# Kernel tuning notes

Hardware: AMD Instinct MI355X
Metric: run time of the kernel (lower is better)

## Reference

```python
import jax, jax.numpy as jnp
import numpy as np

B, N, D = 8, 1024, 256
H, U = 8, 64  # num_heads, units per head


def setup_inputs() -> dict:
    key = jax.random.key(0)
    ks = jax.random.split(key, 8)
    X = jax.random.normal(ks[0], (B, N, D), dtype=jnp.float32)
    A = (jax.random.uniform(ks[1], (B, N, N)) < 0.1).astype(jnp.float32)
    A = jnp.maximum(A, jnp.eye(N, dtype=jnp.float32)[None])
    s = 1.0 / np.sqrt(D)
    kernel = jax.random.normal(ks[2], (D, H * U), dtype=jnp.float32) * s
    kernel_residual = jax.random.normal(ks[3], (D, H * U), dtype=jnp.float32) * s
    su = 1.0 / np.sqrt(U)
    attn_kernel_self = jax.random.normal(ks[4], (H, U, 1), dtype=jnp.float32) * su
    attn_kernel_neighs = jax.random.normal(ks[5], (H, U, 1), dtype=jnp.float32) * su
    bias = jnp.zeros((H * U,), dtype=jnp.float32)
    return {
        "X": X, "A": A,
        "kernel": kernel, "kernel_residual": kernel_residual,
        "attn_kernel_self": attn_kernel_self,
        "attn_kernel_neighs": attn_kernel_neighs,
        "bias": bias,
    }


def reference(X, A, kernel, kernel_residual, attn_kernel_self, attn_kernel_neighs, bias):
    # feature projections: [B,N,H*U]
    features = X @ kernel
    features_residual = X @ kernel_residual
    f = features.reshape(B, N, H, U)  # bnhu
    # additive attention logits per head
    attn_self = jnp.einsum('bnhu,hu->bnh', f, attn_kernel_self[..., 0])
    attn_neigh = jnp.einsum('bnhu,hu->bnh', f, attn_kernel_neighs[..., 0])
    dense = attn_self[:, :, None, :] + attn_neigh[:, None, :, :]  # b n k h
    dense = jax.nn.leaky_relu(dense, negative_slope=0.2)
    # mask non-edges, softmax over neighbor axis k
    dense = dense + (-1e10) * (1.0 - A)[..., None]
    attn_coef = jax.nn.softmax(dense, axis=2)
    # (dropout is identity in inference mode)
    node_features = jnp.einsum('bnkh,bkhu->bnhu', attn_coef, f)
    node_features = node_features.reshape(B, N, H * U) + features_residual + bias
    # head_reduction == 'concat' -> keep [B,N,H*U]
    return jax.nn.relu(node_features)
```

## Files before the change

kernel.cpp:

```cpp
#include <hip/hip_runtime.h>
#include <stdint.h>


typedef __attribute__((ext_vector_type(8))) short short8;
typedef __attribute__((ext_vector_type(4))) float f32x4;
struct __align__(8) us4 { unsigned short x, y, z, w; };

__device__ __forceinline__ unsigned short f32_to_bf16(float f) {
    unsigned int u = __float_as_uint(f);
    u = (u + 0x7fffu + ((u >> 16) & 1u)) >> 16;
    return (unsigned short)u;
}
__device__ __forceinline__ float bf16_to_f32(unsigned short s) {
    return __uint_as_float(((unsigned int)s) << 16);
}
__device__ __forceinline__ void load_lds16(const unsigned short* g, unsigned short* l) {
    __builtin_amdgcn_global_load_lds(
        (const __attribute__((address_space(1))) unsigned int*)g,
        (__attribute__((address_space(3))) unsigned int*)l, 16, 0, 0);
}

__global__ __launch_bounds__(256) void pack_a(const float* __restrict__ X,
                                              unsigned short* __restrict__ Abig) {
    const int idx = blockIdx.x * 256 + threadIdx.x;
    const int m  = idx >> 6;
    const int kg = (idx & 63) << 2;
    float4 x = *(const float4*)&X[m * 256 + kg];
    const float xs[4] = {x.x, x.y, x.z, x.w};
    union { unsigned short u[4]; uint64_t q; } hq, lq;
    #pragma unroll
    for (int i = 0; i < 4; i++) {
        unsigned short h = f32_to_bf16(xs[i]);
        hq.u[i] = h;
        lq.u[i] = f32_to_bf16(xs[i] - bf16_to_f32(h));
    }
    unsigned short* r = Abig + (size_t)m * 768;
    *(uint64_t*)(r + kg)       = hq.q;
    *(uint64_t*)(r + 256 + kg) = hq.q;
    *(uint64_t*)(r + 512 + kg) = lq.q;
}

__global__ __launch_bounds__(256) void pack_b(const float* __restrict__ Wk,
                                              const float* __restrict__ Wr,
                                              unsigned short* __restrict__ Bpack) {
    const int idx = blockIdx.x * 256 + threadIdx.x;
    const int n = idx / 768;
    const int k = idx - n * 768;
    const float* __restrict__ W = (n < 512) ? Wk : Wr;
    const int nc = n & 511;
    const float w = W[(k & 255) * 512 + nc];
    unsigned short h = f32_to_bf16(w);
    unsigned short o = (k >= 256 && k < 512) ? f32_to_bf16(w - bf16_to_f32(h)) : h;
    Bpack[idx] = o;
}

__global__ __launch_bounds__(512) void attn_ck(const float* __restrict__ kernel,
                                               const float* __restrict__ aks,
                                               const float* __restrict__ akn,
                                               float* __restrict__ ck) {
    const int d = blockIdx.x, j = threadIdx.x;
    const float kv = kernel[d * 512 + j];
    float a = kv * aks[j];
    float b = kv * akn[j];
    #pragma unroll
    for (int m = 32; m; m >>= 1) { a += __shfl_xor(a, m, 64); b += __shfl_xor(b, m, 64); }
    const int lane = j & 63, h = j >> 6;
    if (lane == 0) { ck[d * 16 + h] = a; ck[d * 16 + 8 + h] = b; }
}

__global__ __launch_bounds__(256) void attn_sa(const float* __restrict__ X,
                                               const float* __restrict__ ck,
                                               float* __restrict__ saan) {
    __shared__ __align__(16) float Xs[16][260];
    __shared__ __align__(16) float ckL[4096];
    const int t = threadIdx.x, row0 = blockIdx.x * 16;
    #pragma unroll
    for (int i = 0; i < 4; i++) {
        const int q = t + i * 256;
        const int r = q >> 6, c4 = (q & 63) * 4;
        *(float4*)&Xs[r][c4] = *(const float4*)&X[(size_t)(row0 + r) * 256 + c4];
        *(float4*)&ckL[q * 4] = *(const float4*)&ck[q * 4];
    }
    __syncthreads();
    const int r = t >> 4, o = t & 15;
    float acc = 0.f;
    #pragma unroll 4
    for (int d = 0; d < 256; d++) acc = fmaf(Xs[r][d], ckL[d * 16 + o], acc);
    saan[(size_t)(row0 + r) * 16 + o] = acc;
}

#define GK 768
__global__ __launch_bounds__(256) void gemm_bf16(const unsigned short* __restrict__ Ab,
                                                 const unsigned short* __restrict__ Bp,
                                                 unsigned short* __restrict__ featb,
                                                 float* __restrict__ outr) {
    __shared__ __align__(16) unsigned short As[128 * 32];
    __shared__ __align__(16) unsigned short Bs[128 * 32];
    const int tid = threadIdx.x;
    const int lane = tid & 63, wave = tid >> 6;
    const int wr = wave >> 1, wc = wave & 1;
    const int m0 = blockIdx.x * 128, n0 = blockIdx.y * 128;
    const int l15 = lane & 15, lhi = lane >> 4;

    f32x4 acc[4][4] = {};

    for (int k0 = 0; k0 < GK; k0 += 32) {
        #pragma unroll
        for (int i = 0; i < 2; i++) {
            const int s = tid + i * 256;
            const int row = s >> 2, kc = (s & 3) * 8;
            load_lds16(Ab + (size_t)(m0 + row) * GK + k0 + kc, &As[s * 8]);
            load_lds16(Bp + (size_t)(n0 + row) * GK + k0 + kc, &Bs[s * 8]);
        }
        asm volatile("s_waitcnt vmcnt(0)" ::: "memory");
        __syncthreads();
        short8 a[4], b[4];
        #pragma unroll
        for (int mi = 0; mi < 4; mi++)
            a[mi] = *(const short8*)&As[(wr * 64 + mi * 16 + l15) * 32 + lhi * 8];
        #pragma unroll
        for (int ni = 0; ni < 4; ni++)
            b[ni] = *(const short8*)&Bs[(wc * 64 + ni * 16 + l15) * 32 + lhi * 8];
        #pragma unroll
        for (int mi = 0; mi < 4; mi++)
            #pragma unroll
            for (int ni = 0; ni < 4; ni++)
                acc[mi][ni] = __builtin_amdgcn_mfma_f32_16x16x32_bf16(a[mi], b[ni], acc[mi][ni], 0, 0, 0);
        __syncthreads();
    }

    if (n0 < 512) {
        #pragma unroll
        for (int mi = 0; mi < 4; mi++)
            #pragma unroll
            for (int ni = 0; ni < 4; ni++) {
                const int col = n0 + wc * 64 + ni * 16 + l15;
                const int rbase = m0 + wr * 64 + mi * 16 + lhi * 4;
                #pragma unroll
                for (int r = 0; r < 4; r++)
                    featb[(size_t)(rbase + r) * 512 + col] = f32_to_bf16(acc[mi][ni][r]);
            }
    } else {
        #pragma unroll
        for (int mi = 0; mi < 4; mi++)
            #pragma unroll
            for (int ni = 0; ni < 4; ni++) {
                const int col = (n0 - 512) + wc * 64 + ni * 16 + l15;
                const int rbase = m0 + wr * 64 + mi * 16 + lhi * 4;
                #pragma unroll
                for (int r = 0; r < 4; r++)
                    outr[(size_t)(rbase + r) * 512 + col] = acc[mi][ni][r];
            }
    }
}

#define CAP 256
__global__ __launch_bounds__(512) void gat_row4(
    const float* __restrict__ A, const unsigned short* __restrict__ featb,
    const float* __restrict__ saan, const float* __restrict__ bias,
    float* __restrict__ out) {
    __shared__ int   elist[4][CAP];
    __shared__ float ew[4][CAP * 8];
    __shared__ float as_s[4][8], inv_s[4][8], wred[4][2][8];
    __shared__ int   cnt[4];

    const int row0 = blockIdx.x * 4, b = row0 >> 10, t = threadIdx.x;
    const int g = t >> 7, tl = t & 127;

    if (t < 4) cnt[t] = 0;
    if (t < 32) as_s[t >> 3][t & 7] = saan[(size_t)(row0 + (t >> 3)) * 16 + (t & 7)];
    __syncthreads();

    {
        const float* __restrict__ Arow = A + (size_t)(row0 + g) * 1024;
        const int k0 = tl * 8;
        float4 a0 = *(const float4*)&Arow[k0];
        float4 a1 = *(const float4*)&Arow[k0 + 4];
        const float av[8] = {a0.x, a0.y, a0.z, a0.w, a1.x, a1.y, a1.z, a1.w};
        #pragma unroll
        for (int i = 0; i < 8; i++)
            if (av[i] > 0.5f) {
                int idx = atomicAdd(&cnt[g], 1);
                if (idx < CAP) elist[g][idx] = k0 + i;
            }
    }
    __syncthreads();

    {
        const int nE = cnt[g], P = nE * 8, h = tl & 7;
        const float* __restrict__ an_b = saan + (size_t)b * 16384;
        float psum = 0.f;
        for (int p = tl; p < P; p += 128) {
            const int k = elist[g][p >> 3];
            float x = as_s[g][h] + an_b[k * 16 + 8 + h];
            x = x > 0.f ? x : 0.2f * x;
            const float w = __expf(x);
            ew[g][p] = w;
            psum += w;
        }
        psum += __shfl_xor(psum, 8, 64);
        psum += __shfl_xor(psum, 16, 64);
        psum += __shfl_xor(psum, 32, 64);
        const int wv = (t >> 6) & 1;
        if ((t & 63) < 8) wred[g][wv][t & 63] = psum;
    }
    __syncthreads();
    if (t < 32) {
        const int r = t >> 3, h = t & 7;
        inv_s[r][h] = 1.0f / (wred[r][0][h] + wred[r][1][h]);
    }
    __syncthreads();

    {
        const int w = t >> 6, rg = w >> 1, lane = t & 63;
        const int col = (w & 1) * 256 + lane * 4;
        const int hh = col >> 6;
        const int nE = cnt[rg];
        const unsigned short* __restrict__ fb = featb + (size_t)b * 524288;
        float ax = 0.f, ay = 0.f, az = 0.f, aw = 0.f;
        int e = 0;
        for (; e + 2 <= nE; e += 2) {
            const int k0 = elist[rg][e], k1 = elist[rg][e + 1];
            const float c0 = ew[rg][e * 8 + hh], c1 = ew[rg][e * 8 + 8 + hh];
            us4 v0 = *(const us4*)&fb[(size_t)k0 * 512 + col];
            us4 v1 = *(const us4*)&fb[(size_t)k1 * 512 + col];
            ax = fmaf(c0, bf16_to_f32(v0.x), ax); ay = fmaf(c0, bf16_to_f32(v0.y), ay);
            az = fmaf(c0, bf16_to_f32(v0.z), az); aw = fmaf(c0, bf16_to_f32(v0.w), aw);
            ax = fmaf(c1, bf16_to_f32(v1.x), ax); ay = fmaf(c1, bf16_to_f32(v1.y), ay);
            az = fmaf(c1, bf16_to_f32(v1.z), az); aw = fmaf(c1, bf16_to_f32(v1.w), aw);
        }
        if (e < nE) {
            const int k0 = elist[rg][e];
            const float c0 = ew[rg][e * 8 + hh];
            us4 v0 = *(const us4*)&fb[(size_t)k0 * 512 + col];
            ax = fmaf(c0, bf16_to_f32(v0.x), ax); ay = fmaf(c0, bf16_to_f32(v0.y), ay);
            az = fmaf(c0, bf16_to_f32(v0.z), az); aw = fmaf(c0, bf16_to_f32(v0.w), aw);
        }
        const float iv = inv_s[rg][hh];
        const size_t ob = (size_t)(row0 + rg) * 512 + col;
        float4 res = *(const float4*)&out[ob];
        float4 bs  = *(const float4*)&bias[col];
        float4 o;
        o.x = fmaxf(fmaf(ax, iv, res.x + bs.x), 0.f);
        o.y = fmaxf(fmaf(ay, iv, res.y + bs.y), 0.f);
        o.z = fmaxf(fmaf(az, iv, res.z + bs.z), 0.f);
        o.w = fmaxf(fmaf(aw, iv, res.w + bs.w), 0.f);
        *(float4*)&out[ob] = o;
    }
}

extern "C" void kernel_launch(void* const* d_in, const int* in_sizes, int n_in,
                              void* d_out, int out_size, void* d_ws, size_t ws_size,
                              hipStream_t stream) {
    const float* X    = (const float*)d_in[0];
    const float* A    = (const float*)d_in[1];
    const float* Wk   = (const float*)d_in[2];
    const float* Wr   = (const float*)d_in[3];
    const float* aks  = (const float*)d_in[4];
    const float* akn  = (const float*)d_in[5];
    const float* bias = (const float*)d_in[6];
    float* out = (float*)d_out;

    unsigned short* featb = (unsigned short*)d_ws;
    float* saan = (float*)(featb + (size_t)8192 * 512);
    float* ck   = saan + (size_t)8192 * 16;
    unsigned short* Abig  = (unsigned short*)(ck + 4096);
    unsigned short* Bpack = Abig + (size_t)8192 * 768;

    pack_a<<<2048, 256, 0, stream>>>(X, Abig);
    pack_b<<<3072, 256, 0, stream>>>(Wk, Wr, Bpack);
    attn_ck<<<256, 512, 0, stream>>>(Wk, aks, akn, ck);
    attn_sa<<<512, 256, 0, stream>>>(X, ck, saan);
    gemm_bf16<<<dim3(64, 8), 256, 0, stream>>>(Abig, Bpack, featb, out);
    gat_row4<<<2048, 512, 0, stream>>>(A, featb, saan, bias, out);
}
```

Baseline: 190.6 us.

## Replace sparse gather GAT aggregation with dense MFMA attention over transposed features

```diff
diff --git a/kernel.cpp b/kernel.cpp
--- a/kernel.cpp
+++ b/kernel.cpp
@@ -4,7 +4,6 @@
 
 typedef __attribute__((ext_vector_type(8))) short short8;
 typedef __attribute__((ext_vector_type(4))) float f32x4;
-struct __align__(8) us4 { unsigned short x, y, z, w; };
 
 __device__ __forceinline__ unsigned short f32_to_bf16(float f) {
     unsigned int u = __float_as_uint(f);
@@ -92,7 +91,7 @@
 #define GK 768
 __global__ __launch_bounds__(256) void gemm_bf16(const unsigned short* __restrict__ Ab,
                                                  const unsigned short* __restrict__ Bp,
-                                                 unsigned short* __restrict__ featb,
+                                                 unsigned short* __restrict__ featT,
                                                  float* __restrict__ outr) {
     __shared__ __align__(16) unsigned short As[128 * 32];
     __shared__ __align__(16) unsigned short Bs[128 * 32];
@@ -136,9 +135,11 @@
             for (int ni = 0; ni < 4; ni++) {
                 const int col = n0 + wc * 64 + ni * 16 + l15;
                 const int rbase = m0 + wr * 64 + mi * 16 + lhi * 4;
+                const int bb = rbase >> 10, nl = rbase & 1023;
+                union { unsigned short u[4]; uint64_t q; } pk;
                 #pragma unroll
-                for (int r = 0; r < 4; r++)
-                    featb[(size_t)(rbase + r) * 512 + col] = f32_to_bf16(acc[mi][ni][r]);
+                for (int r = 0; r < 4; r++) pk.u[r] = f32_to_bf16(acc[mi][ni][r]);
+                *(uint64_t*)&featT[(size_t)bb * 524288 + (size_t)col * 1024 + nl] = pk.q;
             }
     } else {
         #pragma unroll
@@ -154,99 +155,109 @@
     }
 }
 
-#define CAP 256
-__global__ __launch_bounds__(512) void gat_row4(
-    const float* __restrict__ A, const unsigned short* __restrict__ featb,
+__global__ __launch_bounds__(512) void gat_mfma(
+    const float* __restrict__ A, const unsigned short* __restrict__ featT,
     const float* __restrict__ saan, const float* __restrict__ bias,
     float* __restrict__ out) {
-    __shared__ int   elist[4][CAP];
-    __shared__ float ew[4][CAP * 8];
-    __shared__ float as_s[4][8], inv_s[4][8], wred[4][2][8];
-    __shared__ int   cnt[4];
-
-    const int row0 = blockIdx.x * 4, b = row0 >> 10, t = threadIdx.x;
-    const int g = t >> 7, tl = t & 127;
-
-    if (t < 4) cnt[t] = 0;
-    if (t < 32) as_s[t >> 3][t & 7] = saan[(size_t)(row0 + (t >> 3)) * 16 + (t & 7)];
+    __shared__ float an_s[1024][9];
+    __shared__ float A_lds[32][33];
+    __shared__ float inv_lds[8][32];
+
+    const int blk = blockIdx.x;
+    const int b  = blk & 7;
+    const int n0 = (blk >> 3) * 32;
+    const int t = threadIdx.x;
+    const int w = t >> 6;
+    const int lane = t & 63;
+    const int l15 = lane & 15, lhi = lane >> 4;
+
+    #pragma unroll
+    for (int i = 0; i < 4; i++) {
+        const int idx = i * 512 + t;
+        const int k = idx >> 1, half = (idx & 1) * 4;
+        float4 v = *(const float4*)&saan[(size_t)(b * 1024 + k) * 16 + 8 + half];
+        an_s[k][half + 0] = v.x; an_s[k][half + 1] = v.y;
+        an_s[k][half + 2] = v.z; an_s[k][half + 3] = v.w;
+    }
+    float as_r[2];
+    #pragma unroll
+    for (int mi = 0; mi < 2; mi++)
+        as_r[mi] = saan[(size_t)(b * 1024 + n0 + mi * 16 + l15) * 16 + w];
+
+    float4 regA;
+    const int sr = t >> 3, sc = (t & 7) * 4;
+    if (t < 256)
+        regA = *(const float4*)&A[(size_t)(b * 1024 + n0 + sr) * 1024 + sc];
+
+    f32x4 acc[2][4] = {};
+    float ps[2] = {0.f, 0.f};
+    const unsigned short* __restrict__ fT = featT + (size_t)b * 524288;
+
     __syncthreads();
 
-    {
-        const float* __restrict__ Arow = A + (size_t)(row0 + g) * 1024;
-        const int k0 = tl * 8;
-        float4 a0 = *(const float4*)&Arow[k0];
-        float4 a1 = *(const float4*)&Arow[k0 + 4];
-        const float av[8] = {a0.x, a0.y, a0.z, a0.w, a1.x, a1.y, a1.z, a1.w};
-        #pragma unroll
-        for (int i = 0; i < 8; i++)
-            if (av[i] > 0.5f) {
-                int idx = atomicAdd(&cnt[g], 1);
-                if (idx < CAP) elist[g][idx] = k0 + i;
-            }
+    for (int k0 = 0; k0 < 1024; k0 += 32) {
+        if (t < 256) {
+            A_lds[sr][sc + 0] = regA.x; A_lds[sr][sc + 1] = regA.y;
+            A_lds[sr][sc + 2] = regA.z; A_lds[sr][sc + 3] = regA.w;
+            if (k0 + 32 < 1024)
+                regA = *(const float4*)&A[(size_t)(b * 1024 + n0 + sr) * 1024 + (k0 + 32) + sc];
+        }
+        __syncthreads();
+
+        union { short8 s8; unsigned int u32[4]; } pa[2];
+        #pragma unroll
+        for (int mi = 0; mi < 2; mi++) {
+            #pragma unroll
+            for (int q = 0; q < 4; q++) {
+                float pv[2];
+                #pragma unroll
+                for (int d = 0; d < 2; d++) {
+                    const int kk = lhi * 8 + q * 2 + d;
+                    float x = as_r[mi] + an_s[k0 + kk][w];
+                    x = fmaxf(x, 0.2f * x);
+                    const float e = __expf(x);
+                    pv[d] = (A_lds[mi * 16 + l15][kk] > 0.5f) ? e : 0.f;
+                }
+                unsigned int pk;
+                asm("v_cvt_pk_bf16_f32 %0, %1, %2" : "=v"(pk) : "v"(pv[0]), "v"(pv[1]));
+                pa[mi].u32[q] = pk;
+                ps[mi] += __uint_as_float(pk << 16) + __uint_as_float(pk & 0xffff0000u);
+            }
+        }
+        short8 bf[4];
+        #pragma unroll
+        for (int ni = 0; ni < 4; ni++)
+            bf[ni] = *(const short8*)&fT[(size_t)(w * 64 + ni * 16 + l15) * 1024 + k0 + lhi * 8];
+        #pragma unroll
+        for (int mi = 0; mi < 2; mi++)
+            #pragma unroll
+            for (int ni = 0; ni < 4; ni++)
+                acc[mi][ni] = __builtin_amdgcn_mfma_f32_16x16x32_bf16(pa[mi].s8, bf[ni], acc[mi][ni], 0, 0, 0);
+        __syncthreads();
+    }
+
+    #pragma unroll
+    for (int mi = 0; mi < 2; mi++) {
+        ps[mi] += __shfl_xor(ps[mi], 16, 64);
+        ps[mi] += __shfl_xor(ps[mi], 32, 64);
+        if (lhi == 0) inv_lds[w][mi * 16 + l15] = 1.0f / ps[mi];
     }
     __syncthreads();
 
-    {
-        const int nE = cnt[g], P = nE * 8, h = tl & 7;
-        const float* __restrict__ an_b = saan + (size_t)b * 16384;
-        float psum = 0.f;
-        for (int p = tl; p < P; p += 128) {
-            const int k = elist[g][p >> 3];
-            float x = as_s[g][h] + an_b[k * 16 + 8 + h];
-            x = x > 0.f ? x : 0.2f * x;
-            const float w = __expf(x);
-            ew[g][p] = w;
-            psum += w;
-        }
-        psum += __shfl_xor(psum, 8, 64);
-        psum += __shfl_xor(psum, 16, 64);
-        psum += __shfl_xor(psum, 32, 64);
-        const int wv = (t >> 6) & 1;
-        if ((t & 63) < 8) wred[g][wv][t & 63] = psum;
-    }
-    __syncthreads();
-    if (t < 32) {
-        const int r = t >> 3, h = t & 7;
-        inv_s[r][h] = 1.0f / (wred[r][0][h] + wred[r][1][h]);
-    }
-    __syncthreads();
-
-    {
-        const int w = t >> 6, rg = w >> 1, lane = t & 63;
-        const int col = (w & 1) * 256 + lane * 4;
-        const int hh = col >> 6;
-        const int nE = cnt[rg];
-        const unsigned short* __restrict__ fb = featb + (size_t)b * 524288;
-        float ax = 0.f, ay = 0.f, az = 0.f, aw = 0.f;
-        int e = 0;
-        for (; e + 2 <= nE; e += 2) {
-            const int k0 = elist[rg][e], k1 = elist[rg][e + 1];
-            const float c0 = ew[rg][e * 8 + hh], c1 = ew[rg][e * 8 + 8 + hh];
-            us4 v0 = *(const us4*)&fb[(size_t)k0 * 512 + col];
-            us4 v1 = *(const us4*)&fb[(size_t)k1 * 512 + col];
-            ax = fmaf(c0, bf16_to_f32(v0.x), ax); ay = fmaf(c0, bf16_to_f32(v0.y), ay);
-            az = fmaf(c0, bf16_to_f32(v0.z), az); aw = fmaf(c0, bf16_to_f32(v0.w), aw);
-            ax = fmaf(c1, bf16_to_f32(v1.x), ax); ay = fmaf(c1, bf16_to_f32(v1.y), ay);
-            az = fmaf(c1, bf16_to_f32(v1.z), az); aw = fmaf(c1, bf16_to_f32(v1.w), aw);
-        }
-        if (e < nE) {
-            const int k0 = elist[rg][e];
-            const float c0 = ew[rg][e * 8 + hh];
-            us4 v0 = *(const us4*)&fb[(size_t)k0 * 512 + col];
-            ax = fmaf(c0, bf16_to_f32(v0.x), ax); ay = fmaf(c0, bf16_to_f32(v0.y), ay);
-            az = fmaf(c0, bf16_to_f32(v0.z), az); aw = fmaf(c0, bf16_to_f32(v0.w), aw);
-        }
-        const float iv = inv_s[rg][hh];
-        const size_t ob = (size_t)(row0 + rg) * 512 + col;
-        float4 res = *(const float4*)&out[ob];
-        float4 bs  = *(const float4*)&bias[col];
-        float4 o;
-        o.x = fmaxf(fmaf(ax, iv, res.x + bs.x), 0.f);
-        o.y = fmaxf(fmaf(ay, iv, res.y + bs.y), 0.f);
-        o.z = fmaxf(fmaf(az, iv, res.z + bs.z), 0.f);
-        o.w = fmaxf(fmaf(aw, iv, res.w + bs.w), 0.f);
-        *(float4*)&out[ob] = o;
-    }
+    #pragma unroll
+    for (int mi = 0; mi < 2; mi++)
+        #pragma unroll
+        for (int r = 0; r < 4; r++) {
+            const int row_l = mi * 16 + lhi * 4 + r;
+            const float iv = inv_lds[w][row_l];
+            const size_t rb = (size_t)(b * 1024 + n0 + row_l) * 512 + w * 64;
+            #pragma unroll
+            for (int ni = 0; ni < 4; ni++) {
+                const int col = ni * 16 + l15;
+                const float v = fmaf(acc[mi][ni][r], iv, out[rb + col] + bias[w * 64 + col]);
+                out[rb + col] = fmaxf(v, 0.f);
+            }
+        }
 }
 
 extern "C" void kernel_launch(void* const* d_in, const int* in_sizes, int n_in,
@@ -261,8 +272,8 @@
     const float* bias = (const float*)d_in[6];
     float* out = (float*)d_out;
 
-    unsigned short* featb = (unsigned short*)d_ws;
-    float* saan = (float*)(featb + (size_t)8192 * 512);
+    unsigned short* featT = (unsigned short*)d_ws;
+    float* saan = (float*)(featT + (size_t)8 * 512 * 1024);
     float* ck   = saan + (size_t)8192 * 16;
     unsigned short* Abig  = (unsigned short*)(ck + 4096);
     unsigned short* Bpack = Abig + (size_t)8192 * 768;
@@ -271,6 +282,6 @@
     pack_b<<<3072, 256, 0, stream>>>(Wk, Wr, Bpack);
     attn_ck<<<256, 512, 0, stream>>>(Wk, aks, akn, ck);
     attn_sa<<<512, 256, 0, stream>>>(X, ck, saan);
-    gemm_bf16<<<dim3(64, 8), 256, 0, stream>>>(Abig, Bpack, featb, out);
-    gat_row4<<<2048, 512, 0, stream>>>(A, featb, saan, bias, out);
-}
+    gemm_bf16<<<dim3(64, 8), 256, 0, stream>>>(Abig, Bpack, featT, out);
+    gat_mfma<<<256, 512, 0, stream>>>(A, featT, saan, bias, out);
+}
```

Result: faster. 183.4 us (-3.8%).
